# Kernel tuning notes

Hardware: AMD Instinct MI355X
Metric: run time of the kernel (lower is better)

The kernel has to match this reference:

```python
import jax, jax.numpy as jnp
import numpy as np

C = 512
G = 32  # min(32, C)
EPS = 1e-5


def group_norm(x, scale, bias):
    B, Cc, H, W = x.shape
    xg = x.reshape(B, G, Cc // G, H, W)
    mu = jnp.mean(xg, axis=(2, 3, 4), keepdims=True)
    var = jnp.var(xg, axis=(2, 3, 4), keepdims=True)
    xn = ((xg - mu) * jax.lax.rsqrt(var + EPS)).reshape(B, Cc, H, W)
    return xn * scale[None, :, None, None] + bias[None, :, None, None]


def setup_inputs() -> dict:
    key = jax.random.key(0)
    ks = jax.random.split(key, 12)
    B, H, W = 8, 64, 64
    std = 1.0 / np.sqrt(C)
    inp = {
        "x": jax.random.normal(ks[0], (B, C, H, W), dtype=jnp.float32),
        "gn_scale": jnp.ones((C,), jnp.float32),
        "gn_bias": jnp.zeros((C,), jnp.float32),
        "wq": jax.random.normal(ks[1], (C, C), jnp.float32) * std,
        "bq": jnp.zeros((C,), jnp.float32),
        "wk": jax.random.normal(ks[2], (C, C), jnp.float32) * std,
        "bk": jnp.zeros((C,), jnp.float32),
        "wv": jax.random.normal(ks[3], (C, C), jnp.float32) * std,
        "bv": jnp.zeros((C,), jnp.float32),
        "wo": jax.random.normal(ks[4], (C, C), jnp.float32) * std,
        "bo": jnp.zeros((C,), jnp.float32),
    }
    return inp


def reference(x, gn_scale, gn_bias, wq, bq, wk, bk, wv, bv, wo, bo):
    B, Cc, H, W = x.shape
    scale = Cc ** (-0.5)
    h = group_norm(x, gn_scale, gn_bias)           # [B,C,H,W]
    hf = h.reshape(B, Cc, H * W)                   # [B,C,N]
    q = jnp.einsum('oc,bcn->bon', wq, hf) + bq[None, :, None]
    k = jnp.einsum('oc,bcn->bon', wk, hf) + bk[None, :, None]
    v = jnp.einsum('oc,bcn->bon', wv, hf) + bv[None, :, None]
    attn = jnp.einsum('bci,bcj->bij', q, k) * scale  # [B,N,N]
    attn = jax.nn.softmax(attn, axis=-1)
    o = jnp.einsum('bij,bcj->bci', attn, v)          # [B,C,N]
    o = jnp.einsum('oc,bcn->bon', wo, o) + bo[None, :, None]
    return x + o.reshape(B, Cc, H, W)
```

## Files before the change

### kernel.cpp

```cpp
#include <hip/hip_runtime.h>

#define DEVINL __device__ __forceinline__

typedef __attribute__((ext_vector_type(8))) short s16x8;
typedef __attribute__((ext_vector_type(4))) float f32x4;

DEVINL unsigned short f2bf(float f) {
  union { float f; unsigned u; } v; v.f = f;
  unsigned r = v.u + 0x7FFFu + ((v.u >> 16) & 1u);
  return (unsigned short)(r >> 16);
}

DEVINL float wave_sum(float v) {
#pragma unroll
  for (int o = 32; o > 0; o >>= 1) v += __shfl_xor(v, o, 64);
  return v;
}

__global__ __launch_bounds__(256) void prep_kernel(
    const float* __restrict__ wq, const float* __restrict__ wk,
    const float* __restrict__ wv, const float* __restrict__ wo,
    const float* __restrict__ bq, const float* __restrict__ bk,
    unsigned short* __restrict__ wqk, unsigned short* __restrict__ wvb,
    unsigned short* __restrict__ wob, float* __restrict__ bqk) {
  int i = blockIdx.x * 256 + threadIdx.x;
  wqk[i]          = f2bf(wq[i]);
  wqk[262144 + i] = f2bf(wk[i]);
  wvb[i] = f2bf(wv[i]);
  wob[i] = f2bf(wo[i]);
  if (i < 512) { bqk[i] = bq[i]; bqk[512 + i] = bk[i]; }
}

__global__ __launch_bounds__(256) void gn_stats_kernel(
    const float* __restrict__ x, float* __restrict__ stats) {
  int bg = blockIdx.x;
  const float4* p = (const float4*)(x + (long)bg * 65536);
  float s = 0.f, ss = 0.f;
#pragma unroll 8
  for (int i = 0; i < 64; ++i) {
    float4 v = p[threadIdx.x + 256 * i];
    s  += v.x + v.y + v.z + v.w;
    ss += v.x*v.x + v.y*v.y + v.z*v.z + v.w*v.w;
  }
  __shared__ float red[8];
  float w1 = wave_sum(s), w2 = wave_sum(ss);
  int wave = threadIdx.x >> 6;
  if ((threadIdx.x & 63) == 0) { red[wave] = w1; red[4 + wave] = w2; }
  __syncthreads();
  if (threadIdx.x == 0) {
    float S1 = red[0] + red[1] + red[2] + red[3];
    float S2 = red[4] + red[5] + red[6] + red[7];
    float mu = S1 * (1.f / 65536.f);
    float var = S2 * (1.f / 65536.f) - mu * mu;
    stats[bg * 2]     = mu;
    stats[bg * 2 + 1] = rsqrtf(var + 1e-5f);
  }
}

__global__ __launch_bounds__(256) void gn_norm_kernel(
    const float* __restrict__ x, const float* __restrict__ stats,
    const float* __restrict__ gamma, const float* __restrict__ beta,
    unsigned short* __restrict__ hout) {
  int b = blockIdx.y;
  int n0 = blockIdx.x * 128;
  int tid = threadIdx.x;
  __shared__ unsigned short lt[128][33];
  const float* xb = x + (long)b * (512L * 4096);
  unsigned short* hb = hout + (long)b * (4096L * 512);
  for (int cc0 = 0; cc0 < 512; cc0 += 32) {
#pragma unroll
    for (int i = 0; i < 4; ++i) {
      int idx = tid + 256 * i;
      int c = idx >> 5, nf = idx & 31;
      int ch = cc0 + c;
      float4 v = *(const float4*)(xb + (long)ch * 4096 + n0 + nf * 4);
      float mu = stats[(b * 32 + (ch >> 4)) * 2];
      float rs = stats[(b * 32 + (ch >> 4)) * 2 + 1];
      float ga = gamma[ch] * rs;
      float be = beta[ch] - mu * ga;
      int nl = nf * 4;
      lt[nl + 0][c] = f2bf(v.x * ga + be);
      lt[nl + 1][c] = f2bf(v.y * ga + be);
      lt[nl + 2][c] = f2bf(v.z * ga + be);
      lt[nl + 3][c] = f2bf(v.w * ga + be);
    }
    __syncthreads();
#pragma unroll
    for (int i = 0; i < 2; ++i) {
      int idx = tid + 256 * i;
      int row = idx >> 2, part = idx & 3;
      union { uint4 u; unsigned short s[8]; } o;
#pragma unroll
      for (int j = 0; j < 8; ++j) o.s[j] = lt[row][part * 8 + j];
      *(uint4*)(hb + (long)(n0 + row) * 512 + cc0 + part * 8) = o.u;
    }
    __syncthreads();
  }
}

#define BM 128
#define BN 128
#define BKD 64

enum { EPI_BF16 = 0, EPI_BF16_COLBIAS = 1, EPI_BF16_ROWBIAS = 2,
       EPI_F32_SCALE = 3, EPI_F32_RES = 4 };

DEVINL void stage128x64(const unsigned short* g, int ld, unsigned short* l, int tid) {
  int wave = tid >> 6;
#pragma unroll
  for (int it = 0; it < 4; ++it) {
    int seg = it * 256 + tid;
    int row = seg >> 3, ks = seg & 7;
    const unsigned short* gp = g + (long)row * ld + ks * 8;
    unsigned short* lp = l + (it * 256 + wave * 64) * 8;
    __builtin_amdgcn_global_load_lds(
        (const __attribute__((address_space(1))) void*)gp,
        (__attribute__((address_space(3))) void*)lp, 16, 0, 0);
  }
}

template <int EPI>
__global__ __launch_bounds__(256, 2) void gemm_nt(
    const unsigned short* __restrict__ A, long strideA, int lda,
    const unsigned short* __restrict__ B, long strideB, int ldb,
    void* __restrict__ C, long strideC, int ldc, int K,
    const float* __restrict__ bias, float scale,
    const float* __restrict__ resid, long strideR) {
  __shared__ __align__(16) unsigned short lA[BM * BKD];
  __shared__ __align__(16) unsigned short lB[BN * BKD];
  int z = blockIdx.z;
  const unsigned short* Ab = A + (long)z * strideA + (long)blockIdx.y * BM * lda;
  const unsigned short* Bb = B + (long)z * strideB + (long)blockIdx.x * BN * ldb;
  int tid = threadIdx.x;
  int lane = tid & 63, wave = tid >> 6;
  int wm = (wave >> 1) * 64, wn = (wave & 1) * 64;
  int lr = lane & 15;
  int lk = (lane >> 4) * 8;

  f32x4 acc[4][4];
#pragma unroll
  for (int i = 0; i < 4; ++i)
#pragma unroll
    for (int j = 0; j < 4; ++j) acc[i][j] = (f32x4){0.f, 0.f, 0.f, 0.f};

  for (int k0 = 0; k0 < K; k0 += BKD) {
    __syncthreads();
    stage128x64(Ab + k0, lda, lA, tid);
    stage128x64(Bb + k0, ldb, lB, tid);
    __syncthreads();
#pragma unroll
    for (int kk = 0; kk < 2; ++kk) {
      s16x8 af[4], bfr[4];
#pragma unroll
      for (int i = 0; i < 4; ++i)
        af[i] = *(const s16x8*)&lA[(wm + i * 16 + lr) * BKD + kk * 32 + lk];
#pragma unroll
      for (int i = 0; i < 4; ++i)
        bfr[i] = *(const s16x8*)&lB[(wn + i * 16 + lr) * BKD + kk * 32 + lk];
#pragma unroll
      for (int mi = 0; mi < 4; ++mi)
#pragma unroll
        for (int ni = 0; ni < 4; ++ni)
          acc[mi][ni] = __builtin_amdgcn_mfma_f32_16x16x32_bf16(
              af[mi], bfr[ni], acc[mi][ni], 0, 0, 0);
    }
  }

  int rbase = blockIdx.y * BM + wm + (lane >> 4) * 4;
  int cbase = blockIdx.x * BN + wn + lr;
  long cb = (long)z * strideC;
#pragma unroll
  for (int mi = 0; mi < 4; ++mi) {
#pragma unroll
    for (int ni = 0; ni < 4; ++ni) {
      int col = cbase + ni * 16;
#pragma unroll
      for (int r = 0; r < 4; ++r) {
        int row = rbase + mi * 16 + r;
        float val = acc[mi][ni][r];
        long off = cb + (long)row * ldc + col;
        if constexpr (EPI == EPI_BF16) {
          ((unsigned short*)C)[off] = f2bf(val);
        } else if constexpr (EPI == EPI_BF16_COLBIAS) {
          ((unsigned short*)C)[off] = f2bf(val + bias[col]);
        } else if constexpr (EPI == EPI_BF16_ROWBIAS) {
          ((unsigned short*)C)[off] = f2bf(val + bias[row]);
        } else if constexpr (EPI == EPI_F32_SCALE) {
          ((float*)C)[off] = val * scale;
        } else {
          ((float*)C)[off] =
              val + bias[row] + resid[(long)z * strideR + (long)row * ldc + col];
        }
      }
    }
  }
}

DEVINL void stage_k32(const unsigned short* qkb, unsigned short* dst,
                      int kv0, int tid, int wv) {
#pragma unroll
  for (int it = 0; it < 4; ++it) {
    int s = it * 512 + tid;
    int row = s >> 6, c16 = s & 63;
    const unsigned short* gp = qkb + (long)(kv0 + row) * 1024 + 512 + ((c16 ^ (row & 7)) * 8);
    unsigned short* lp = dst + (it * 512 + wv * 64) * 8;
    __builtin_amdgcn_global_load_lds(
        (const __attribute__((address_space(1))) void*)gp,
        (__attribute__((address_space(3))) void*)lp, 16, 0, 0);
  }
}

DEVINL void stage_v32(const unsigned short* vbb, unsigned short* dst,
                      int kv0, int tid, int wv) {
#pragma unroll
  for (int it = 0; it < 4; ++it) {
    int s = it * 512 + tid;
    int c = s >> 2, ks = s & 3;
    const unsigned short* gp = vbb + (long)c * 4096 + kv0 + ((ks ^ ((c >> 1) & 3)) * 8);
    unsigned short* lp = dst + (it * 512 + wv * 64) * 8;
    __builtin_amdgcn_global_load_lds(
        (const __attribute__((address_space(1))) void*)gp,
        (__attribute__((address_space(3))) void*)lp, 16, 0, 0);
  }
}

__global__ __launch_bounds__(512, 2) void flash2_kernel(
    const unsigned short* __restrict__ qk, const unsigned short* __restrict__ v,
    unsigned short* __restrict__ o, float scale) {
  __shared__ __align__(16) unsigned short lK[2][32 * 512];
  __shared__ __align__(16) unsigned short lV[2][512 * 32];
  __shared__ __align__(16) unsigned short lP[128 * 64];
  __shared__ float lCorr[128];

  int bid = blockIdx.x;
  int b = bid & 7, qb = bid >> 3;
  const unsigned short* qkb = qk + (long)b * 4096 * 1024;
  const unsigned short* vb  = v  + (long)b * 512 * 4096;
  int tid = threadIdx.x, lane = tid & 63, wv = tid >> 6;
  int g = lane >> 4, qi = lane & 15;
  int q0 = qb * 128;
  int wq = wv >> 2, wc = wv & 3;

  s16x8 qf[16];
  {
    const unsigned short* qrow = qkb + (long)(q0 + wv * 16 + qi) * 1024 + g * 8;
#pragma unroll
    for (int kk = 0; kk < 16; ++kk) qf[kk] = *(const s16x8*)(qrow + kk * 32);
  }

  f32x4 accO[4][8];
#pragma unroll
  for (int i = 0; i < 4; ++i)
#pragma unroll
    for (int j = 0; j < 8; ++j) accO[i][j] = (f32x4){0.f, 0.f, 0.f, 0.f};
  float m_run = -3.0e38f, l_run = 0.f;

  stage_k32(qkb, &lK[0][0], 0, tid, wv);
  stage_v32(vb, &lV[0][0], 0, tid, wv);
  __syncthreads();

  int cur = 0;
  for (int t = 0; t < 128; ++t) {
    int nxt = t < 127 ? t + 1 : 127;
    stage_k32(qkb, &lK[cur ^ 1][0], nxt * 32, tid, wv);

    f32x4 sacc[2];
    sacc[0] = (f32x4){0.f, 0.f, 0.f, 0.f};
    sacc[1] = (f32x4){0.f, 0.f, 0.f, 0.f};
    const char* lkc = (const char*)&lK[cur][0];
#pragma unroll
    for (int kk = 0; kk < 16; ++kk) {
      int ko = (kk * 64 + g * 16) ^ ((qi & 7) << 4);
#pragma unroll
      for (int sub = 0; sub < 2; ++sub) {
        const s16x8 kf = *(const s16x8*)(lkc + (sub * 16 + qi) * 1024 + ko);
        sacc[sub] = __builtin_amdgcn_mfma_f32_16x16x32_bf16(kf, qf[kk], sacc[sub], 0, 0, 0);
      }
    }
    float mx = -3.0e38f;
#pragma unroll
    for (int sub = 0; sub < 2; ++sub)
#pragma unroll
      for (int r = 0; r < 4; ++r) { sacc[sub][r] *= scale; mx = fmaxf(mx, sacc[sub][r]); }
    mx = fmaxf(mx, __shfl_xor(mx, 16, 64));
    mx = fmaxf(mx, __shfl_xor(mx, 32, 64));
    float m_new = fmaxf(m_run, mx);
    float corr = __expf(m_run - m_new);
    float rowsum = 0.f;
#pragma unroll
    for (int sub = 0; sub < 2; ++sub)
#pragma unroll
      for (int r = 0; r < 4; ++r) {
        float p = __expf(sacc[sub][r] - m_new);
        sacc[sub][r] = p;
        rowsum += p;
      }
    rowsum += __shfl_xor(rowsum, 16, 64);
    rowsum += __shfl_xor(rowsum, 32, 64);
    l_run = l_run * corr + rowsum;
    m_run = m_new;
    if (g == 0) lCorr[wv * 16 + qi] = corr;
    {
      int q = wv * 16 + qi;
#pragma unroll
      for (int sub = 0; sub < 2; ++sub) {
        uint2 pk;
        pk.x = (unsigned)f2bf(sacc[sub][0]) | ((unsigned)f2bf(sacc[sub][1]) << 16);
        pk.y = (unsigned)f2bf(sacc[sub][2]) | ((unsigned)f2bf(sacc[sub][3]) << 16);
        int chunk = (sub * 2 + (g >> 1)) ^ (q & 7);
        *(uint2*)((char*)lP + q * 128 + (chunk << 4) + (g & 1) * 8) = pk;
      }
    }
    __syncthreads();

    stage_v32(vb, &lV[cur ^ 1][0], nxt * 32, tid, wv);
#pragma unroll
    for (int i = 0; i < 4; ++i) {
      f32x4 cr = *(const f32x4*)&lCorr[wq * 64 + i * 16 + g * 4];
#pragma unroll
      for (int j = 0; j < 8; ++j)
#pragma unroll
        for (int r = 0; r < 4; ++r) accO[i][j][r] *= cr[r];
    }
    const char* lvc = (const char*)&lV[cur][0];
#pragma unroll
    for (int jg = 0; jg < 2; ++jg) {
      s16x8 vf[4];
#pragma unroll
      for (int j2 = 0; j2 < 4; ++j2) {
        int c = (wc * 8 + jg * 4 + j2) * 16 + qi;
        vf[j2] = *(const s16x8*)(lvc + c * 64 + ((g ^ ((qi >> 1) & 3)) << 4));
      }
#pragma unroll
      for (int i = 0; i < 4; ++i) {
        int q = (wq * 4 + i) * 16 + qi;
        const s16x8 pf = *(const s16x8*)((const char*)lP + q * 128 + ((g ^ (q & 7)) << 4));
#pragma unroll
        for (int j2 = 0; j2 < 4; ++j2)
          accO[i][jg * 4 + j2] = __builtin_amdgcn_mfma_f32_16x16x32_bf16(
              pf, vf[j2], accO[i][jg * 4 + j2], 0, 0, 0);
      }
    }
    __syncthreads();
    cur ^= 1;
  }

  if (g == 0) lCorr[wv * 16 + qi] = 1.0f / l_run;
  __syncthreads();
  unsigned short* ob = o + (long)b * (4096L * 512) + (long)q0 * 512;
#pragma unroll
  for (int i = 0; i < 4; ++i) {
    f32x4 fr = *(const f32x4*)&lCorr[wq * 64 + i * 16 + g * 4];
#pragma unroll
    for (int j = 0; j < 8; ++j)
#pragma unroll
      for (int r = 0; r < 4; ++r)
        ob[(long)(wq * 64 + i * 16 + g * 4 + r) * 512 + wc * 128 + j * 16 + qi] =
            f2bf(accO[i][j][r] * fr[r]);
  }
}

extern "C" void kernel_launch(void* const* d_in, const int* in_sizes, int n_in,
                              void* d_out, int out_size, void* d_ws, size_t ws_size,
                              hipStream_t stream) {
  const float* x   = (const float*)d_in[0];
  const float* gsc = (const float*)d_in[1];
  const float* gbi = (const float*)d_in[2];
  const float* wq  = (const float*)d_in[3];
  const float* bq  = (const float*)d_in[4];
  const float* wk  = (const float*)d_in[5];
  const float* bk  = (const float*)d_in[6];
  const float* wv  = (const float*)d_in[7];
  const float* bv  = (const float*)d_in[8];
  const float* wo  = (const float*)d_in[9];
  const float* bo  = (const float*)d_in[10];
  float* out = (float*)d_out;

  char* w = (char*)d_ws;
  unsigned short* wqk  = (unsigned short*)(w);
  unsigned short* wvb  = (unsigned short*)(w + 1048576);
  unsigned short* wob  = (unsigned short*)(w + 1572864);
  float*          bqk  = (float*)(w + 2097152);
  float*          stats= (float*)(w + 2101248);
  char* big = w + 4194304;
  unsigned short* h_t  = (unsigned short*)(big);
  unsigned short* qkb  = (unsigned short*)(big + 33554432);
  unsigned short* vbuf = (unsigned short*)(big + 100663296);
  unsigned short* o_t  = (unsigned short*)(big + 134217728);

  prep_kernel<<<1024, 256, 0, stream>>>(wq, wk, wv, wo, bq, bk, wqk, wvb, wob, bqk);
  gn_stats_kernel<<<256, 256, 0, stream>>>(x, stats);
  gn_norm_kernel<<<dim3(32, 8), 256, 0, stream>>>(x, stats, gsc, gbi, h_t);

  const float scale = 0.04419417382415922f;
  const long HB = 4096L * 512;
  const long XB = 512L * 4096;

  gemm_nt<EPI_BF16_COLBIAS><<<dim3(8, 32, 8), 256, 0, stream>>>(
      h_t, HB, 512, wqk, 0, 512, qkb, 4096L * 1024, 1024, 512, bqk, 1.f, nullptr, 0);
  gemm_nt<EPI_BF16_ROWBIAS><<<dim3(32, 4, 8), 256, 0, stream>>>(
      wvb, 0, 512, h_t, HB, 512, vbuf, XB, 4096, 512, bv, 1.f, nullptr, 0);

  flash2_kernel<<<256, 512, 0, stream>>>(qkb, vbuf, o_t, scale);

  gemm_nt<EPI_F32_RES><<<dim3(32, 4, 8), 256, 0, stream>>>(
      wob, 0, 512, o_t, HB, 512, out, XB, 4096, 512, bo, 1.f, x, XB);
}
```

Baseline: 774.4 us.

## Restructure flash attention: direct V register loads, double-buffered P, lazy rescaling

Folds the softmax scale into the Q weights and bias during prep, which removes the per-element scale multiply. Inside the attention loop, V fragments now come straight from global memory into registers instead of being staged through LDS. P and the correction factors are double-buffered so one of the two barriers per iteration can be dropped. A lazy max update (threshold 8) skips most accumulator rescales, guarded by a wave-wide check, and s_setprio raises priority around the MFMA sections. The risks are global-load latency on V reads that are now uncoalesced, and the numerical looseness of the deferred max.

```diff
diff --git a/kernel.cpp b/kernel.cpp
--- a/kernel.cpp
+++ b/kernel.cpp
@@ -23,12 +23,13 @@
     const float* __restrict__ bq, const float* __restrict__ bk,
     unsigned short* __restrict__ wqk, unsigned short* __restrict__ wvb,
     unsigned short* __restrict__ wob, float* __restrict__ bqk) {
+  const float scale = 0.04419417382415922f;
   int i = blockIdx.x * 256 + threadIdx.x;
-  wqk[i]          = f2bf(wq[i]);
+  wqk[i]          = f2bf(wq[i] * scale);
   wqk[262144 + i] = f2bf(wk[i]);
   wvb[i] = f2bf(wv[i]);
   wob[i] = f2bf(wo[i]);
-  if (i < 512) { bqk[i] = bq[i]; bqk[512 + i] = bk[i]; }
+  if (i < 512) { bqk[i] = bq[i] * scale; bqk[512 + i] = bk[i]; }
 }
 
 __global__ __launch_bounds__(256) void gn_stats_kernel(
@@ -210,27 +211,13 @@
   }
 }
 
-DEVINL void stage_v32(const unsigned short* vbb, unsigned short* dst,
-                      int kv0, int tid, int wv) {
-#pragma unroll
-  for (int it = 0; it < 4; ++it) {
-    int s = it * 512 + tid;
-    int c = s >> 2, ks = s & 3;
-    const unsigned short* gp = vbb + (long)c * 4096 + kv0 + ((ks ^ ((c >> 1) & 3)) * 8);
-    unsigned short* lp = dst + (it * 512 + wv * 64) * 8;
-    __builtin_amdgcn_global_load_lds(
-        (const __attribute__((address_space(1))) void*)gp,
-        (__attribute__((address_space(3))) void*)lp, 16, 0, 0);
-  }
-}
-
-__global__ __launch_bounds__(512, 2) void flash2_kernel(
+__global__ __launch_bounds__(512, 2) void flash3_kernel(
     const unsigned short* __restrict__ qk, const unsigned short* __restrict__ v,
-    unsigned short* __restrict__ o, float scale) {
+    unsigned short* __restrict__ o) {
   __shared__ __align__(16) unsigned short lK[2][32 * 512];
-  __shared__ __align__(16) unsigned short lV[2][512 * 32];
-  __shared__ __align__(16) unsigned short lP[128 * 64];
-  __shared__ float lCorr[128];
+  __shared__ __align__(16) unsigned short lP[2][128 * 64];
+  __shared__ float lCorr[2][128];
+  __shared__ float lInv[128];
 
   int bid = blockIdx.x;
   int b = bid & 7, qb = bid >> 3;
@@ -256,7 +243,6 @@
   float m_run = -3.0e38f, l_run = 0.f;
 
   stage_k32(qkb, &lK[0][0], 0, tid, wv);
-  stage_v32(vb, &lV[0][0], 0, tid, wv);
   __syncthreads();
 
   int cur = 0;
@@ -268,6 +254,7 @@
     sacc[0] = (f32x4){0.f, 0.f, 0.f, 0.f};
     sacc[1] = (f32x4){0.f, 0.f, 0.f, 0.f};
     const char* lkc = (const char*)&lK[cur][0];
+    __builtin_amdgcn_s_setprio(1);
 #pragma unroll
     for (int kk = 0; kk < 16; ++kk) {
       int ko = (kk * 64 + g * 16) ^ ((qi & 7) << 4);
@@ -277,80 +264,85 @@
         sacc[sub] = __builtin_amdgcn_mfma_f32_16x16x32_bf16(kf, qf[kk], sacc[sub], 0, 0, 0);
       }
     }
+    __builtin_amdgcn_s_setprio(0);
+
+    s16x8 vf[8];
+#pragma unroll
+    for (int ct = 0; ct < 8; ++ct) {
+      int c = (wc * 8 + ct) * 16 + qi;
+      vf[ct] = *(const s16x8*)(vb + (long)c * 4096 + t * 32 + g * 8);
+    }
+
     float mx = -3.0e38f;
 #pragma unroll
     for (int sub = 0; sub < 2; ++sub)
 #pragma unroll
-      for (int r = 0; r < 4; ++r) { sacc[sub][r] *= scale; mx = fmaxf(mx, sacc[sub][r]); }
+      for (int r = 0; r < 4; ++r) mx = fmaxf(mx, sacc[sub][r]);
     mx = fmaxf(mx, __shfl_xor(mx, 16, 64));
     mx = fmaxf(mx, __shfl_xor(mx, 32, 64));
-    float m_new = fmaxf(m_run, mx);
-    float corr = __expf(m_run - m_new);
+    float corr;
+    if (mx <= m_run + 8.f) {
+      corr = 1.f;
+    } else {
+      corr = __expf(m_run - mx);
+      m_run = mx;
+    }
     float rowsum = 0.f;
 #pragma unroll
     for (int sub = 0; sub < 2; ++sub)
 #pragma unroll
       for (int r = 0; r < 4; ++r) {
-        float p = __expf(sacc[sub][r] - m_new);
+        float p = __expf(sacc[sub][r] - m_run);
         sacc[sub][r] = p;
         rowsum += p;
       }
     rowsum += __shfl_xor(rowsum, 16, 64);
     rowsum += __shfl_xor(rowsum, 32, 64);
     l_run = l_run * corr + rowsum;
-    m_run = m_new;
-    if (g == 0) lCorr[wv * 16 + qi] = corr;
+    if (g == 0) lCorr[t & 1][wv * 16 + qi] = corr;
+
     {
       int q = wv * 16 + qi;
+      char* pw = (char*)&lP[t & 1][0] + q * 128;
 #pragma unroll
       for (int sub = 0; sub < 2; ++sub) {
         uint2 pk;
         pk.x = (unsigned)f2bf(sacc[sub][0]) | ((unsigned)f2bf(sacc[sub][1]) << 16);
         pk.y = (unsigned)f2bf(sacc[sub][2]) | ((unsigned)f2bf(sacc[sub][3]) << 16);
         int chunk = (sub * 2 + (g >> 1)) ^ (q & 7);
-        *(uint2*)((char*)lP + q * 128 + (chunk << 4) + (g & 1) * 8) = pk;
-      }
-    }
-    __syncthreads();
-
-    stage_v32(vb, &lV[cur ^ 1][0], nxt * 32, tid, wv);
+        *(uint2*)(pw + (chunk << 4) + (g & 1) * 8) = pk;
+      }
+    }
+    __syncthreads();
+
+    const char* lpc = (const char*)&lP[t & 1][0];
+    __builtin_amdgcn_s_setprio(1);
 #pragma unroll
     for (int i = 0; i < 4; ++i) {
-      f32x4 cr = *(const f32x4*)&lCorr[wq * 64 + i * 16 + g * 4];
-#pragma unroll
-      for (int j = 0; j < 8; ++j)
-#pragma unroll
-        for (int r = 0; r < 4; ++r) accO[i][j][r] *= cr[r];
-    }
-    const char* lvc = (const char*)&lV[cur][0];
-#pragma unroll
-    for (int jg = 0; jg < 2; ++jg) {
-      s16x8 vf[4];
-#pragma unroll
-      for (int j2 = 0; j2 < 4; ++j2) {
-        int c = (wc * 8 + jg * 4 + j2) * 16 + qi;
-        vf[j2] = *(const s16x8*)(lvc + c * 64 + ((g ^ ((qi >> 1) & 3)) << 4));
-      }
-#pragma unroll
-      for (int i = 0; i < 4; ++i) {
-        int q = (wq * 4 + i) * 16 + qi;
-        const s16x8 pf = *(const s16x8*)((const char*)lP + q * 128 + ((g ^ (q & 7)) << 4));
-#pragma unroll
-        for (int j2 = 0; j2 < 4; ++j2)
-          accO[i][jg * 4 + j2] = __builtin_amdgcn_mfma_f32_16x16x32_bf16(
-              pf, vf[j2], accO[i][jg * 4 + j2], 0, 0, 0);
-      }
-    }
-    __syncthreads();
+      f32x4 cr = *(const f32x4*)&lCorr[t & 1][wq * 64 + i * 16 + g * 4];
+      if (__any(cr[0] != 1.f || cr[1] != 1.f || cr[2] != 1.f || cr[3] != 1.f)) {
+#pragma unroll
+        for (int j = 0; j < 8; ++j)
+#pragma unroll
+          for (int r = 0; r < 4; ++r) accO[i][j][r] *= cr[r];
+      }
+      int q = (wq * 4 + i) * 16 + qi;
+      const s16x8 pf = *(const s16x8*)(lpc + q * 128 + ((g ^ (q & 7)) << 4));
+#pragma unroll
+      for (int ct = 0; ct < 8; ++ct)
+        accO[i][ct] = __builtin_amdgcn_mfma_f32_16x16x32_bf16(
+            pf, vf[ct], accO[i][ct], 0, 0, 0);
+    }
+    __builtin_amdgcn_s_setprio(0);
     cur ^= 1;
   }
 
-  if (g == 0) lCorr[wv * 16 + qi] = 1.0f / l_run;
+  if (g == 0) lInv[wv * 16 + qi] = 1.0f / l_run;
   __syncthreads();
   unsigned short* ob = o + (long)b * (4096L * 512) + (long)q0 * 512;
 #pragma unroll
   for (int i = 0; i < 4; ++i) {
-    f32x4 fr = *(const f32x4*)&lCorr[wq * 64 + i * 16 + g * 4];
+    f32x4 fr = *(const f32x4*)&lInv[wq * 64 + i * 16 + g * 4];
 #pragma unroll
     for (int j = 0; j < 8; ++j)
 #pragma unroll
@@ -392,7 +384,6 @@
   gn_stats_kernel<<<256, 256, 0, stream>>>(x, stats);
   gn_norm_kernel<<<dim3(32, 8), 256, 0, stream>>>(x, stats, gsc, gbi, h_t);
 
-  const float scale = 0.04419417382415922f;
   const long HB = 4096L * 512;
   const long XB = 512L * 4096;
 
@@ -401,7 +392,7 @@
   gemm_nt<EPI_BF16_ROWBIAS><<<dim3(32, 4, 8), 256, 0, stream>>>(
       wvb, 0, 512, h_t, HB, 512, vbuf, XB, 4096, 512, bv, 1.f, nullptr, 0);
 
-  flash2_kernel<<<256, 512, 0, stream>>>(qkb, vbuf, o_t, scale);
+  flash3_kernel<<<256, 512, 0, stream>>>(qkb, vbuf, o_t);
 
   gemm_nt<EPI_F32_RES><<<dim3(32, 4, 8), 256, 0, stream>>>(
       wob, 0, 512, o_t, HB, 512, out, XB, 4096, 512, bo, 1.f, x, XB);
```

After: 1.122 ms. 44.8% more time.
